# Kernel optimization log

Hardware: AMD Instinct MI355X
Metric: run time of the kernel (lower is better)

Reference implementation:

```python
import jax, jax.numpy as jnp
import numpy as np

H, DK, DV = 16, 64, 64
PHASE_MAX = 5
TEMP = 5.0
GAMMA = 0.9
BASE = 10000.0

def _rotate_half(x):
    d = x.shape[-1] // 2
    return jnp.concatenate((-x[..., d:], x[..., :d]), axis=-1)

def _inv_freq(dtype):
    return (1.0 / BASE ** (jnp.arange(0, DK, 2, dtype=jnp.float32) / DK)).astype(dtype)

def setup_inputs() -> dict:
    key = jax.random.key(0)
    ks = jax.random.split(key, 6)
    B, T, D = 4, 4096, 2048
    return {
        'hidden_states': jax.random.normal(ks[0], (B, T, D), jnp.float32),
        'W_turn': jax.random.normal(ks[1], (B, H, DV, DK), jnp.float32) * 0.1,
        'q_w': jax.random.normal(ks[2], (H * DK, D), jnp.float32) * 0.02,
        'o_w': jax.random.normal(ks[3], (D, H * DV), jnp.float32) * 0.02,
        'k_w': jax.random.normal(ks[4], (H * DK, D), jnp.float32) * 0.02,
        'v_w': jax.random.normal(ks[5], (H * DV, D), jnp.float32) * 0.02,
        'read_scale': jnp.asarray(-3.0, jnp.float32),
    }

def reference(hidden_states, W_turn, q_w, o_w, k_w, v_w, read_scale):
    B, T, D = hidden_states.shape
    dtype = hidden_states.dtype
    inv_freq = _inv_freq(dtype)

    # ---- read (layer 0) ----
    q = (hidden_states @ q_w.T).reshape(B, T, H, DK).transpose(0, 2, 1, 3)  # (B,H,T,dk)
    qn = jnp.linalg.norm(q, axis=-1, keepdims=True)
    q = q / jnp.maximum(qn, 1e-12)
    P = PHASE_MAX + 1
    phase = jnp.arange(P, dtype=dtype)
    angles = phase[:, None] * inv_freq                      # (P, dk/2)
    cos = jnp.concatenate([jnp.cos(angles)] * 2, axis=-1)   # (P, dk)
    sin = jnp.concatenate([jnp.sin(angles)] * 2, axis=-1)
    cos_b = cos.reshape(P, 1, 1, 1, DK)
    sin_b = sin.reshape(P, 1, 1, 1, DK)
    q_un = q[None]                                          # (P,B,H,T,dk)
    q_all = q_un * cos_b + _rotate_half(q_un) * sin_b
    reads = jnp.einsum('pbhtd,bhvd->pbhtv', q_all, W_turn)  # (P,B,H,T,dv)
    scores = jnp.linalg.norm(reads, axis=-1) / jnp.sqrt(jnp.asarray(DV, dtype))
    alpha = jax.nn.softmax(scores * TEMP, axis=0)           # (P,B,H,T)
    read = jnp.sum(alpha[..., None] * reads, axis=0)        # (B,H,T,dv)
    merged = read.transpose(0, 2, 1, 3).reshape(B, T, H * DV)
    out = hidden_states + jax.nn.sigmoid(read_scale).astype(dtype) * (merged @ o_w.T)

    # ---- write from content (content = hidden_states) ----
    k = (hidden_states @ k_w.T).reshape(B, T, H, DK).transpose(0, 2, 1, 3)
    v = (hidden_states @ v_w.T).reshape(B, T, H, DV).transpose(0, 2, 1, 3)
    kn = jnp.linalg.norm(k, axis=-1, keepdims=True)
    k = k / jnp.maximum(kn, 1e-12)
    residual = jnp.einsum('bhtv,bhtd->bhvd', v, k) / max(T, 1)
    cos1 = jnp.concatenate([jnp.cos(inv_freq)] * 2, axis=-1)  # 1-step aging
    sin1 = jnp.concatenate([jnp.sin(inv_freq)] * 2, axis=-1)
    W_aged = W_turn * cos1 + _rotate_half(W_turn) * sin1
    W_new = GAMMA * W_aged + residual
    return out, W_new
```

## Files before the change

kernel.cpp:

```cpp
#include <hip/hip_runtime.h>
#include <math.h>

typedef unsigned short u16;
typedef __bf16 bf16x8 __attribute__((ext_vector_type(8)));
typedef float f32x4 __attribute__((ext_vector_type(4)));

typedef __attribute__((address_space(1))) const void gas_t;
typedef __attribute__((address_space(3))) void las_t;

__device__ __forceinline__ void async16(const void* g, void* l) {
    __builtin_amdgcn_global_load_lds((gas_t*)g, (las_t*)l, 16, 0, 0);
}

__device__ __forceinline__ float b2f(u16 u) {
    union { unsigned u; float f; } c; c.u = ((unsigned)u) << 16; return c.f;
}
__device__ __forceinline__ u16 f2b(float f) {
    union { float f; unsigned u; } c; c.f = f;
    unsigned x = c.u + 0x7FFFu + ((c.u >> 16) & 1u);
    return (u16)(x >> 16);
}

__global__ __launch_bounds__(256)
void cvt_kernel(const float* __restrict__ in, u16* __restrict__ out, int n4) {
    int i = blockIdx.x * 256 + threadIdx.x;
    int stride = gridDim.x * 256;
    for (; i < n4; i += stride) {
        float4 f = ((const float4*)in)[i];
        ushort4 u;
        u.x = f2b(f.x); u.y = f2b(f.y); u.z = f2b(f.z); u.w = f2b(f.w);
        ((ushort4*)out)[i] = u;
    }
}

__global__ __launch_bounds__(256)
void cvt3_kernel(const float* __restrict__ a, const float* __restrict__ b,
                 const float* __restrict__ c, u16* __restrict__ out) {
    int i = blockIdx.x * 256 + threadIdx.x;
    int seg = i / 524288, off = i - seg * 524288;
    const float* src = (seg == 0) ? a : (seg == 1) ? b : c;
    float4 f = ((const float4*)src)[off];
    ushort4 u;
    u.x = f2b(f.x); u.y = f2b(f.y); u.z = f2b(f.z); u.w = f2b(f.w);
    ((ushort4*)out)[i] = u;
}

__global__ __launch_bounds__(256)
void wprep_kernel(const float* __restrict__ W, u16* __restrict__ wp) {
    int idx = blockIdx.x * 256 + threadIdx.x;
    int d = idx & 63;
    int v = (idx >> 6) & 63;
    int p = (idx >> 12) % 6;
    int bh = idx / 24576;
    const float* Wb = W + (((size_t)bh * 64 + v) << 6);
    float invf = expf(-(float)(d & 31) * (9.210340371976184f / 32.f));
    float ang = (float)p * invf;
    float c = cosf(ang), s = sinf(ang);
    float rot = (d < 32) ? Wb[d + 32] : -Wb[d - 32];
    wp[idx] = f2b(c * Wb[d] + s * rot);
}

template<int MODE>
__global__ __launch_bounds__(512, 2)
void gemm_bt256(const u16* __restrict__ A, const u16* __restrict__ Bw,
                int M, int N, int K,
                u16* __restrict__ obf, const float* __restrict__ resid,
                float* __restrict__ of32, const float* __restrict__ scale_ptr) {
    __shared__ __align__(16) u16 lsA[2][256 * 64];
    __shared__ __align__(16) u16 lsB[2][256 * 64];
    const int tid = threadIdx.x;
    const int lane = tid & 63;
    const int wm = (tid >> 6) >> 2;
    const int wn = (tid >> 6) & 3;
    const int nbx = N >> 8;

    int bid = blockIdx.x;
    const int cpx = gridDim.x >> 3;
    bid = (bid & 7) * cpx + (bid >> 3);
    const int m0 = (bid / nbx) << 8;
    const int n0 = (bid % nbx) << 8;

    f32x4 acc[8][4];
#pragma unroll
    for (int i = 0; i < 8; ++i)
#pragma unroll
        for (int j = 0; j < 4; ++j) acc[i][j] = (f32x4){0.f, 0.f, 0.f, 0.f};

    const int srow = tid >> 3;
    const int sslot = (tid & 7) ^ (srow & 7);
    const char* Ab = (const char*)A;
    const char* Bb = (const char*)Bw;
    const int nkt = K >> 6;

    auto stage = [&](int buf, int kt) {
        const int k0 = kt << 6;
#pragma unroll
        for (int i = 0; i < 4; ++i) {
            int rowA = m0 + i * 64 + srow;
            async16(Ab + ((size_t)rowA * K + k0) * 2 + (sslot << 4),
                    (char*)&lsA[buf][0] + i * 8192 + tid * 16);
            int rowB = n0 + i * 64 + srow;
            async16(Bb + ((size_t)rowB * K + k0) * 2 + (sslot << 4),
                    (char*)&lsB[buf][0] + i * 8192 + tid * 16);
        }
    };

    stage(0, 0);
    __syncthreads();
    int cur = 0;
    for (int kt = 0; kt < nkt; ++kt) {
        if (kt + 1 < nkt) stage(cur ^ 1, kt + 1);
#pragma unroll
        for (int kk = 0; kk < 2; ++kk) {
            const int kb = kk * 64 + ((lane >> 4) << 4);
            bf16x8 af[8], bf[4];
#pragma unroll
            for (int m = 0; m < 8; ++m) {
                int row = wm * 128 + m * 16 + (lane & 15);
                af[m] = *(const bf16x8*)((const char*)&lsA[cur][0] + row * 128 + (kb ^ ((row & 7) << 4)));
            }
#pragma unroll
            for (int n = 0; n < 4; ++n) {
                int row = wn * 64 + n * 16 + (lane & 15);
                bf[n] = *(const bf16x8*)((const char*)&lsB[cur][0] + row * 128 + (kb ^ ((row & 7) << 4)));
            }
            __builtin_amdgcn_s_setprio(1);
#pragma unroll
            for (int m = 0; m < 8; ++m)
#pragma unroll
                for (int n = 0; n < 4; ++n)
                    acc[m][n] = __builtin_amdgcn_mfma_f32_16x16x32_bf16(bf[n], af[m], acc[m][n], 0, 0, 0);
            __builtin_amdgcn_s_setprio(0);
        }
        __syncthreads();
        cur ^= 1;
    }

    float sig = 0.f;
    if (MODE == 1) sig = 1.f / (1.f + expf(-scale_ptr[0]));

    const int crow = wm * 128 + (lane & 15);
    const int ccol0 = wn * 64 + ((lane >> 4) << 2);
#pragma unroll
    for (int m = 0; m < 8; ++m) {
#pragma unroll
        for (int n = 0; n < 4; ++n) {
            size_t gi = (size_t)(m0 + crow + m * 16) * N + (n0 + ccol0 + n * 16);
            if (MODE == 0) {
                ushort4 u;
                u.x = f2b(acc[m][n][0]); u.y = f2b(acc[m][n][1]);
                u.z = f2b(acc[m][n][2]); u.w = f2b(acc[m][n][3]);
                *(ushort4*)&obf[gi] = u;
            } else {
                float4 rv = *(const float4*)&resid[gi];
                float4 o;
                o.x = rv.x + sig * acc[m][n][0];
                o.y = rv.y + sig * acc[m][n][1];
                o.z = rv.z + sig * acc[m][n][2];
                o.w = rv.w + sig * acc[m][n][3];
                *(float4*)&of32[gi] = o;
            }
        }
    }
}

__global__ __launch_bounds__(256)
void reads_kernel(const u16* __restrict__ qkv, const u16* __restrict__ wp,
                  u16* __restrict__ merged) {
    __shared__ __align__(16) u16 lsW[384 * 64];
    const int tid = threadIdx.x, lane = tid & 63, w = tid >> 6;
    const int bh = blockIdx.x, tc = blockIdx.y;
    const int b = bh >> 4, h = bh & 15;

    const char* src = (const char*)(wp + (size_t)bh * 24576);
#pragma unroll
    for (int it = 0; it < 12; ++it) {
        int x = (it * 256 + tid) << 4;
        int row = x >> 7;
        int wb = x & 127;
        *(uint4*)((char*)lsW + x) = *(const uint4*)(src + row * 128 + (wb ^ ((row & 7) << 4)));
    }
    __syncthreads();

    for (int tt = 0; tt < 4; ++tt) {
        const int t0 = tc * 256 + tt * 64 + w * 16;
        const size_t qoff = ((size_t)b * 4096 + t0 + (lane & 15)) * 3072 + h * 64 + ((lane >> 4) << 3);
        uint4 a0u = *(const uint4*)&qkv[qoff];
        uint4 a1u = *(const uint4*)&qkv[qoff + 32];

        float ss = 0.f;
        {
            unsigned a[8] = {a0u.x, a0u.y, a0u.z, a0u.w, a1u.x, a1u.y, a1u.z, a1u.w};
#pragma unroll
            for (int i = 0; i < 8; ++i) {
                union { unsigned u; float f; } lo, hi;
                lo.u = a[i] << 16; hi.u = a[i] & 0xFFFF0000u;
                ss += lo.f * lo.f + hi.f * hi.f;
            }
        }
        ss += __shfl_xor(ss, 16);
        ss += __shfl_xor(ss, 32);
        float sc = 1.0f / fmaxf(sqrtf(ss), 1e-12f);

        bf16x8 a0 = __builtin_bit_cast(bf16x8, a0u);
        bf16x8 a1 = __builtin_bit_cast(bf16x8, a1u);

        f32x4 acc[24];
#pragma unroll
        for (int i = 0; i < 24; ++i) acc[i] = (f32x4){0.f, 0.f, 0.f, 0.f};
#pragma unroll
        for (int kk = 0; kk < 2; ++kk) {
            bf16x8 a = kk ? a1 : a0;
            const int kb = kk * 64 + ((lane >> 4) << 4);
#pragma unroll
            for (int nf = 0; nf < 24; ++nf) {
                int row = nf * 16 + (lane & 15);
                bf16x8 bb = *(const bf16x8*)((const char*)lsW + row * 128 + (kb ^ ((row & 7) << 4)));
                acc[nf] = __builtin_amdgcn_mfma_f32_16x16x32_bf16(bb, a, acc[nf], 0, 0, 0);
            }
        }

        float alpha[6];
#pragma unroll
        for (int p = 0; p < 6; ++p) {
            float x = 0.f;
#pragma unroll
            for (int fv = 0; fv < 4; ++fv) {
                f32x4 v = acc[p * 4 + fv];
#pragma unroll
                for (int r = 0; r < 4; ++r) x += v[r] * v[r];
            }
            x += __shfl_xor(x, 16);
            x += __shfl_xor(x, 32);
            alpha[p] = sqrtf(x) * sc * (5.0f / 8.0f);
        }
        {
            float m = alpha[0];
#pragma unroll
            for (int p = 1; p < 6; ++p) m = fmaxf(m, alpha[p]);
            float s = 0.f;
#pragma unroll
            for (int p = 0; p < 6; ++p) { float e = expf(alpha[p] - m); s += e; alpha[p] = e; }
            float inv = 1.f / s;
#pragma unroll
            for (int p = 0; p < 6; ++p) alpha[p] *= inv;
        }
#pragma unroll
        for (int fv = 0; fv < 4; ++fv) {
            float o[4];
#pragma unroll
            for (int r = 0; r < 4; ++r) {
                float acc_o = 0.f;
#pragma unroll
                for (int p = 0; p < 6; ++p) acc_o += alpha[p] * acc[p * 4 + fv][r];
                o[r] = acc_o * sc;
            }
            size_t gi = ((size_t)b * 4096 + t0 + (lane & 15)) * 1024
                        + h * 64 + fv * 16 + ((lane >> 4) << 2);
            ushort4 u;
            u.x = f2b(o[0]); u.y = f2b(o[1]); u.z = f2b(o[2]); u.w = f2b(o[3]);
            *(ushort4*)&merged[gi] = u;
        }
    }
}

__global__ __launch_bounds__(256)
void resid_mfma(const u16* __restrict__ qkv, float* __restrict__ part) {
    __shared__ __align__(16) u16 kT[64 * 32];
    __shared__ __align__(16) u16 vT[64 * 32];
    const int bh = blockIdx.x, sp = blockIdx.y;
    const int b = bh >> 4, h = bh & 15;
    const int tid = threadIdx.x, lane = tid & 63, wv = tid >> 6;
    const int tl = tid >> 3;
    const int c8 = tid & 7;

    f32x4 acc[4];
#pragma unroll
    for (int dt = 0; dt < 4; ++dt) acc[dt] = (f32x4){0.f, 0.f, 0.f, 0.f};

    const int r15 = lane & 15, g = lane >> 4;
    const int vrow = wv * 16 + r15;
    const int vaddr = vrow * 64 + ((g ^ ((vrow >> 3) & 3)) << 4);
    int kaddr[4];
#pragma unroll
    for (int dt = 0; dt < 4; ++dt) {
        int kr = dt * 16 + r15;
        kaddr[dt] = kr * 64 + ((g ^ ((kr >> 3) & 3)) << 4);
    }

    for (int c = 0; c < 8; ++c) {
        size_t row = ((size_t)b * 4096 + sp * 256 + c * 32 + tl) * 3072 + h * 64 + c8 * 8;
        uint4 kq = *(const uint4*)&qkv[row + 1024];
        uint4 vq = *(const uint4*)&qkv[row + 2048];

        unsigned kw[4] = {kq.x, kq.y, kq.z, kq.w};
        unsigned vw[4] = {vq.x, vq.y, vq.z, vq.w};
        float kf[8];
        float ss = 0.f;
#pragma unroll
        for (int i = 0; i < 4; ++i) {
            union { unsigned u; float f; } lo, hi;
            lo.u = kw[i] << 16; hi.u = kw[i] & 0xFFFF0000u;
            kf[2 * i] = lo.f; kf[2 * i + 1] = hi.f;
            ss += lo.f * lo.f + hi.f * hi.f;
        }
        ss += __shfl_xor(ss, 1);
        ss += __shfl_xor(ss, 2);
        ss += __shfl_xor(ss, 4);
        float sc = 1.0f / fmaxf(sqrtf(ss), 1e-12f);

        const int gt = (tl >> 3), o = (tl & 7);
#pragma unroll
        for (int j = 0; j < 8; ++j) {
            int r = 8 * c8 + j;
            int a = r * 32 + ((gt ^ ((r >> 3) & 3)) * 8 + o);
            kT[a] = f2b(kf[j] * sc);
            vT[a] = (u16)((vw[j >> 1] >> ((j & 1) * 16)) & 0xFFFFu);
        }
        __syncthreads();

        bf16x8 vf = *(const bf16x8*)((const char*)vT + vaddr);
#pragma unroll
        for (int dt = 0; dt < 4; ++dt) {
            bf16x8 knf = *(const bf16x8*)((const char*)kT + kaddr[dt]);
            acc[dt] = __builtin_amdgcn_mfma_f32_16x16x32_bf16(knf, vf, acc[dt], 0, 0, 0);
        }
        __syncthreads();
    }

    float* dst = part + ((size_t)sp * 64 + bh) * 4096 + (size_t)vrow * 64;
#pragma unroll
    for (int dt = 0; dt < 4; ++dt) {
        float4 f4;
        f4.x = acc[dt][0]; f4.y = acc[dt][1]; f4.z = acc[dt][2]; f4.w = acc[dt][3];
        *(float4*)(dst + dt * 16 + g * 4) = f4;
    }
}

__global__ __launch_bounds__(256)
void wnew_kernel(const float* __restrict__ W, const float* __restrict__ part,
                 float* __restrict__ outW) {
    int idx = blockIdx.x * 256 + threadIdx.x;
    int d = idx & 63;
    float w = W[idx];
    float rot = (d < 32) ? -W[idx + 32] : W[idx - 32];
    float invf = expf(-(float)(d & 31) * (9.210340371976184f / 32.f));
    float aged = w * cosf(invf) + rot * sinf(invf);
    float r = 0.f;
#pragma unroll
    for (int s = 0; s < 16; ++s) r += part[(size_t)s * 262144 + idx];
    outW[idx] = 0.9f * aged + r * (1.0f / 4096.0f);
}

extern "C" void kernel_launch(void* const* d_in, const int* in_sizes, int n_in,
                              void* d_out, int out_size, void* d_ws, size_t ws_size,
                              hipStream_t stream) {
    const float* hidden = (const float*)d_in[0];
    const float* Wturn  = (const float*)d_in[1];
    const float* qw     = (const float*)d_in[2];
    const float* ow     = (const float*)d_in[3];
    const float* kw     = (const float*)d_in[4];
    const float* vw     = (const float*)d_in[5];
    const float* rs     = (const float*)d_in[6];
    float* out  = (float*)d_out;
    float* outW = out + 33554432;

    char* ws = (char*)d_ws;
    u16* hid_bf = (u16*)(ws + 0);
    u16* qkv    = (u16*)(ws + 67108864);
    u16* mrg    = (u16*)(ws + 167772160);
    u16* wcat   = (u16*)(ws + 201326592);
    u16* ow_bf  = (u16*)(ws + 213909504);
    u16* wp     = (u16*)(ws + 218103808);
    float* part = (float*)(ws + 222298112);

    cvt_kernel<<<4096, 256, 0, stream>>>(hidden, hid_bf, 33554432 / 4);
    cvt3_kernel<<<6144, 256, 0, stream>>>(qw, kw, vw, wcat);
    cvt_kernel<<<2048, 256, 0, stream>>>(ow, ow_bf, 2097152 / 4);
    wprep_kernel<<<6144, 256, 0, stream>>>(Wturn, wp);

    gemm_bt256<0><<<768, 512, 0, stream>>>(hid_bf, wcat, 16384, 3072, 2048, qkv, nullptr, nullptr, nullptr);

    reads_kernel<<<dim3(64, 16), 256, 0, stream>>>(qkv, wp, mrg);
    gemm_bt256<1><<<512, 512, 0, stream>>>(mrg, ow_bf, 16384, 2048, 1024, nullptr, hidden, out, rs);
    resid_mfma<<<dim3(64, 16), 256, 0, stream>>>(qkv, part);
    wnew_kernel<<<1024, 256, 0, stream>>>(Wturn, part, outW);
}
```

Measured before the change: 466.4 us.

## Shrink GEMM M-tile to 128 and use triple-buffered LDS pipeline

Changes both bf16 GEMMs from 256x256 to 128x256 output tiles and doubles their grid sizes. K-tile staging moves from a double buffer to a three-slot ring with prefetch distance two. The explicit vmcnt waits plus a raw barrier replace the per-iteration __syncthreads. Smaller tiles raise block count for better CU balance but lower the arithmetic intensity per tile. The 3x48KB LDS footprint may still allow two blocks per CU.

```diff
diff --git a/kernel.cpp b/kernel.cpp
--- a/kernel.cpp
+++ b/kernel.cpp
@@ -62,12 +62,11 @@
 
 template<int MODE>
 __global__ __launch_bounds__(512, 2)
-void gemm_bt256(const u16* __restrict__ A, const u16* __restrict__ Bw,
+void gemm_bt128(const u16* __restrict__ A, const u16* __restrict__ Bw,
                 int M, int N, int K,
                 u16* __restrict__ obf, const float* __restrict__ resid,
                 float* __restrict__ of32, const float* __restrict__ scale_ptr) {
-    __shared__ __align__(16) u16 lsA[2][256 * 64];
-    __shared__ __align__(16) u16 lsB[2][256 * 64];
+    __shared__ __align__(16) u16 ls[3][24576];
     const int tid = threadIdx.x;
     const int lane = tid & 63;
     const int wm = (tid >> 6) >> 2;
@@ -77,12 +76,12 @@
     int bid = blockIdx.x;
     const int cpx = gridDim.x >> 3;
     bid = (bid & 7) * cpx + (bid >> 3);
-    const int m0 = (bid / nbx) << 8;
+    const int m0 = (bid / nbx) << 7;
     const int n0 = (bid % nbx) << 8;
 
-    f32x4 acc[8][4];
-#pragma unroll
-    for (int i = 0; i < 8; ++i)
+    f32x4 acc[4][4];
+#pragma unroll
+    for (int i = 0; i < 4; ++i)
 #pragma unroll
         for (int j = 0; j < 4; ++j) acc[i][j] = (f32x4){0.f, 0.f, 0.f, 0.f};
 
@@ -92,57 +91,64 @@
     const char* Bb = (const char*)Bw;
     const int nkt = K >> 6;
 
-    auto stage = [&](int buf, int kt) {
+    auto stage = [&](int slot, int kt) {
         const int k0 = kt << 6;
-#pragma unroll
-        for (int i = 0; i < 4; ++i) {
+        char* base = (char*)&ls[slot][0];
+#pragma unroll
+        for (int i = 0; i < 2; ++i) {
             int rowA = m0 + i * 64 + srow;
             async16(Ab + ((size_t)rowA * K + k0) * 2 + (sslot << 4),
-                    (char*)&lsA[buf][0] + i * 8192 + tid * 16);
+                    base + i * 8192 + tid * 16);
+        }
+#pragma unroll
+        for (int i = 0; i < 4; ++i) {
             int rowB = n0 + i * 64 + srow;
             async16(Bb + ((size_t)rowB * K + k0) * 2 + (sslot << 4),
-                    (char*)&lsB[buf][0] + i * 8192 + tid * 16);
+                    base + 16384 + i * 8192 + tid * 16);
         }
     };
 
     stage(0, 0);
-    __syncthreads();
-    int cur = 0;
+    stage(1, 1);
     for (int kt = 0; kt < nkt; ++kt) {
-        if (kt + 1 < nkt) stage(cur ^ 1, kt + 1);
+        if (kt < nkt - 1) asm volatile("s_waitcnt vmcnt(6)" ::: "memory");
+        else              asm volatile("s_waitcnt vmcnt(0)" ::: "memory");
+        __builtin_amdgcn_s_barrier();
+        if (kt + 2 < nkt) stage((kt + 2) % 3, kt + 2);
+
+        const char* Al = (const char*)&ls[kt % 3][0];
+        const char* Bl = Al + 16384;
 #pragma unroll
         for (int kk = 0; kk < 2; ++kk) {
             const int kb = kk * 64 + ((lane >> 4) << 4);
-            bf16x8 af[8], bf[4];
-#pragma unroll
-            for (int m = 0; m < 8; ++m) {
-                int row = wm * 128 + m * 16 + (lane & 15);
-                af[m] = *(const bf16x8*)((const char*)&lsA[cur][0] + row * 128 + (kb ^ ((row & 7) << 4)));
+            bf16x8 af[4], bf[4];
+#pragma unroll
+            for (int m = 0; m < 4; ++m) {
+                int row = wm * 64 + m * 16 + (lane & 15);
+                af[m] = *(const bf16x8*)(Al + row * 128 + (kb ^ ((row & 7) << 4)));
             }
 #pragma unroll
             for (int n = 0; n < 4; ++n) {
                 int row = wn * 64 + n * 16 + (lane & 15);
-                bf[n] = *(const bf16x8*)((const char*)&lsB[cur][0] + row * 128 + (kb ^ ((row & 7) << 4)));
+                bf[n] = *(const bf16x8*)(Bl + row * 128 + (kb ^ ((row & 7) << 4)));
             }
             __builtin_amdgcn_s_setprio(1);
 #pragma unroll
-            for (int m = 0; m < 8; ++m)
+            for (int m = 0; m < 4; ++m)
 #pragma unroll
                 for (int n = 0; n < 4; ++n)
                     acc[m][n] = __builtin_amdgcn_mfma_f32_16x16x32_bf16(bf[n], af[m], acc[m][n], 0, 0, 0);
             __builtin_amdgcn_s_setprio(0);
         }
-        __syncthreads();
-        cur ^= 1;
     }
 
     float sig = 0.f;
     if (MODE == 1) sig = 1.f / (1.f + expf(-scale_ptr[0]));
 
-    const int crow = wm * 128 + (lane & 15);
+    const int crow = wm * 64 + (lane & 15);
     const int ccol0 = wn * 64 + ((lane >> 4) << 2);
 #pragma unroll
-    for (int m = 0; m < 8; ++m) {
+    for (int m = 0; m < 4; ++m) {
 #pragma unroll
         for (int n = 0; n < 4; ++n) {
             size_t gi = (size_t)(m0 + crow + m * 16) * N + (n0 + ccol0 + n * 16);
@@ -379,10 +385,10 @@
     cvt_kernel<<<2048, 256, 0, stream>>>(ow, ow_bf, 2097152 / 4);
     wprep_kernel<<<6144, 256, 0, stream>>>(Wturn, wp);
 
-    gemm_bt256<0><<<768, 512, 0, stream>>>(hid_bf, wcat, 16384, 3072, 2048, qkv, nullptr, nullptr, nullptr);
+    gemm_bt128<0><<<1536, 512, 0, stream>>>(hid_bf, wcat, 16384, 3072, 2048, qkv, nullptr, nullptr, nullptr);
 
     reads_kernel<<<dim3(64, 16), 256, 0, stream>>>(qkv, wp, mrg);
-    gemm_bt256<1><<<512, 512, 0, stream>>>(mrg, ow_bf, 16384, 2048, 1024, nullptr, hidden, out, rs);
+    gemm_bt128<1><<<1024, 512, 0, stream>>>(mrg, ow_bf, 16384, 2048, 1024, nullptr, hidden, out, rs);
     resid_mfma<<<dim3(64, 16), 256, 0, stream>>>(qkv, part);
     wnew_kernel<<<1024, 256, 0, stream>>>(Wturn, part, outW);
 }
```

Result: no change. 457.4 us (-1.9%).
